# Optimization experiments

Measured on AMD Instinct MI355X. Metric: run time of the kernel, lower is better.

The kernel has to match this reference:

```python
import jax, jax.numpy as jnp
import numpy as np


def setup_inputs() -> dict:
    key = jax.random.key(0)
    k0, k1, k2, k3 = jax.random.split(key, 4)
    B, L, D, H = 8, 4096, 300, 128  # batch, leaves (power of 2), embed dim, hidden
    x = jax.random.normal(k0, (B, L, D), jnp.float32)
    W_leaf = jax.random.normal(k1, (D, 2 * H), jnp.float32) * (1.0 / np.sqrt(D))
    b_leaf = jnp.zeros((2 * H,), jnp.float32)
    W_l = jax.random.normal(k2, (H, 5 * H), jnp.float32) * (1.0 / np.sqrt(H))
    W_r = jax.random.normal(k3, (H, 5 * H), jnp.float32) * (1.0 / np.sqrt(H))
    b = jnp.zeros((5 * H,), jnp.float32)
    return {"x": x, "W_leaf": W_leaf, "b_leaf": b_leaf, "W_l": W_l, "W_r": W_r, "b": b}


def reference(x, W_leaf, b_leaf, W_l, W_r, b):
    """Binary TreeLSTM over a complete tree: leaves -> root.

    x: [B, L, D] leaf embeddings, L a power of 2.
    Leaf transform: linear projection split into (h, c) (SPINN-style).
    REDUCE: 5-gate child-sum-of-two composition.
    Returns root hidden state: [B, H].
    """
    H = W_l.shape[0]
    hc = x @ W_leaf + b_leaf                     # [B, L, 2H]
    h, c = hc[..., :H], hc[..., H:]
    levels = int(np.log2(x.shape[1]))
    for _ in range(levels):                      # level-batched tree reduction
        h_l, h_r = h[:, 0::2], h[:, 1::2]        # [B, n/2, H]
        c_l, c_r = c[:, 0::2], c[:, 1::2]
        gates = h_l @ W_l + h_r @ W_r + b        # [B, n/2, 5H]
        i, fl, fr, o, g = jnp.split(gates, 5, axis=-1)
        c = (jax.nn.sigmoid(fl) * c_l
             + jax.nn.sigmoid(fr) * c_r
             + jax.nn.sigmoid(i) * jnp.tanh(g))
        h = jax.nn.sigmoid(o) * jnp.tanh(c)
    return h[:, 0]                               # root hidden state [B, H]
```

## Files before the change

### kernel.cpp

```cpp
#include <hip/hip_runtime.h>
#include <hip/hip_bf16.h>
#include <math.h>


typedef __attribute__((ext_vector_type(8))) short bfrag8;
typedef __attribute__((ext_vector_type(4))) float f32x4;
typedef __attribute__((ext_vector_type(4))) short s16x4;

__device__ __forceinline__ float sigf(float x) { return 1.0f / (1.0f + __expf(-x)); }
__device__ __forceinline__ short f2bf(float f) {
    __hip_bfloat16 h = __float2bfloat16(f);
    return *reinterpret_cast<short*>(&h);
}
#define GLDS(gp, lp) __builtin_amdgcn_global_load_lds( \
    (const __attribute__((address_space(1))) void*)(gp), \
    (__attribute__((address_space(3))) void*)(lp), 16, 0, 0)

__global__ __launch_bounds__(256) void reorder_kernel(
    const float* __restrict__ W_l, const float* __restrict__ W_r,
    const float* __restrict__ W_leaf,
    short* __restrict__ Wcat_ch, short* __restrict__ Wleaf_ch)
{
    int idx = blockIdx.x * 256 + threadIdx.x;
    if (idx < 163840) {
        int n = idx >> 8, k = idx & 255;
        float v = (k < 128) ? W_l[k * 640 + n] : W_r[(k - 128) * 640 + n];
        Wcat_ch[(((size_t)(k >> 3)) * 640 + n) * 8 + (k & 7)] = f2bf(v);
        return;
    }
    idx -= 163840;
    if (idx < 81920) {
        int n = idx / 320, k = idx - n * 320;
        short v = (k < 300) ? f2bf(W_leaf[k * 256 + n]) : (short)0;
        Wleaf_ch[(((size_t)(k >> 3)) * 256 + n) * 8 + (k & 7)] = v;
    }
}

__global__ __launch_bounds__(256) void convx_kernel(
    const float* __restrict__ x, short* __restrict__ xbf)
{
    __shared__ short Ls[64 * 328];
    const int tid = threadIdx.x;
    const int R0 = blockIdx.x * 64;
    for (int i = tid; i < 64 * 75; i += 256) {
        int r = i / 75, q = i - r * 75;
        f32x4 v = *(const f32x4*)(x + (size_t)(R0 + r) * 300 + q * 4);
        s16x4 o;
        #pragma unroll
        for (int t = 0; t < 4; ++t) o[t] = f2bf(v[t]);
        *(s16x4*)(Ls + r * 328 + q * 4) = o;
    }
    for (int i = tid; i < 64 * 20; i += 256) {
        int r = i / 20, q = i - r * 20;
        Ls[r * 328 + 300 + q] = 0;
    }
    __syncthreads();
    for (int i = tid; i < 40 * 64; i += 256) {
        int c = i >> 6, r = i & 63;
        bfrag8 v = *(const bfrag8*)(Ls + r * 328 + c * 8);
        *(bfrag8*)(xbf + ((size_t)c * 32768 + R0 + r) * 8) = v;
    }
}

__global__ __launch_bounds__(256) void leaf_kernel(
    const short* __restrict__ A, const short* __restrict__ B,
    const float* __restrict__ bleaf,
    short* __restrict__ hD,
    float* __restrict__ cD)
{
    __shared__ short Als[8 * 128 * 8];
    __shared__ short Bls[8 * 128 * 8];
    const int tid  = threadIdx.x;
    const int w    = tid >> 6, lane = tid & 63;
    const int quad = lane >> 4, l16 = lane & 15;
    const int mBlk = blockIdx.x * 128, nBlk = blockIdx.y * 128;
    const int waveM = (w >> 1) * 64, waveN = (w & 1) * 64;

    f32x4 acc[4][4] = {};

    for (int k0 = 0; k0 < 40; k0 += 8) {
        #pragma unroll
        for (int q = 0; q < 4; ++q) {
            int rr = w * 4 + q, cl = rr >> 1, rh = rr & 1;
            GLDS(A + ((size_t)(k0 + cl) * 32768 + mBlk + rh * 64 + lane) * 8,
                 (char*)Als + rr * 1024);
            GLDS(B + ((size_t)(k0 + cl) * 256 + nBlk + rh * 64 + lane) * 8,
                 (char*)Bls + rr * 1024);
        }
        __syncthreads();
        #pragma unroll
        for (int ks = 0; ks < 2; ++ks) {
            int ca = ks * 4 + quad;
            bfrag8 af[4], bf[4];
            #pragma unroll
            for (int i = 0; i < 4; ++i)
                af[i] = *(const bfrag8*)(Als + (ca * 128 + waveM + i * 16 + l16) * 8);
            #pragma unroll
            for (int jn = 0; jn < 4; ++jn)
                bf[jn] = *(const bfrag8*)(Bls + (ca * 128 + waveN + jn * 16 + l16) * 8);
            #pragma unroll
            for (int i = 0; i < 4; ++i)
                #pragma unroll
                for (int jn = 0; jn < 4; ++jn)
                    acc[i][jn] = __builtin_amdgcn_mfma_f32_16x16x32_bf16(
                                     af[i], bf[jn], acc[i][jn], 0, 0, 0);
        }
        __syncthreads();
    }

    #pragma unroll
    for (int i = 0; i < 4; ++i) {
        int row0 = mBlk + waveM + i * 16 + quad * 4;
        #pragma unroll
        for (int jn = 0; jn < 4; ++jn) {
            int col = nBlk + waveN + jn * 16 + l16;
            float bv = bleaf[col];
            #pragma unroll
            for (int rg = 0; rg < 4; ++rg) {
                float v = acc[i][jn][rg] + bv;
                int m = row0 + rg;
                if (nBlk == 0) {
                    int hc = col;
                    hD[(((size_t)((m & 1) * 16 + (hc >> 3))) * 16384 + (m >> 1)) * 8
                       + (hc & 7)] = f2bf(v);
                } else {
                    cD[(size_t)m * 128 + (col - 128)] = v;
                }
            }
        }
    }
}

__global__ __launch_bounds__(256, 2) void level_ws_kernel(
    const short* __restrict__ A,
    const float* __restrict__ cprev,
    const short* __restrict__ Wch,
    const float* __restrict__ bias,
    short* __restrict__ hout, float* __restrict__ cout,
    int M, float* __restrict__ out_final)
{
    __shared__ short Als[32 * 64 * 8];
    const int tid  = threadIdx.x;
    const int w    = tid >> 6, lane = tid & 63;
    const int quad = lane >> 4, l16 = lane & 15;
    const int j  = blockIdx.y;
    const int tb = blockIdx.x * 64;
    const int h  = j * 16 + l16;

    {
        int row = tb + lane; if (row >= M) row = 0;
        #pragma unroll
        for (int s = 0; s < 8; ++s)
            GLDS(A + ((size_t)(s * 4 + w) * M + row) * 8,
                 (char*)Als + (s * 4 + w) * 1024);
    }

    bfrag8 Wfr[5][8];
    #pragma unroll
    for (int g = 0; g < 5; ++g)
        #pragma unroll
        for (int s = 0; s < 8; ++s)
            Wfr[g][s] = *(const bfrag8*)(Wch + ((size_t)(s * 4 + quad) * 640
                                                + g * 128 + h) * 8);
    const float bi  = bias[h],       bfl = bias[128 + h], bfr_ = bias[256 + h];
    const float bo  = bias[384 + h], bg  = bias[512 + h];

    __syncthreads();

    f32x4 acc[5] = {};
    #pragma unroll
    for (int s = 0; s < 8; ++s) {
        bfrag8 af = *(const bfrag8*)(Als + ((s * 4 + quad) * 64 + w * 16 + l16) * 8);
        #pragma unroll
        for (int g = 0; g < 5; ++g)
            acc[g] = __builtin_amdgcn_mfma_f32_16x16x32_bf16(af, Wfr[g][s], acc[g], 0, 0, 0);
    }

    const int Mn = M >> 1;
    #pragma unroll
    for (int rg = 0; rg < 4; ++rg) {
        int m = tb + w * 16 + quad * 4 + rg;
        if (m < M) {
            float gi  = acc[0][rg] + bi;
            float gfl = acc[1][rg] + bfl;
            float gfr = acc[2][rg] + bfr_;
            float go  = acc[3][rg] + bo;
            float gg  = acc[4][rg] + bg;
            float cl  = cprev[(size_t)(2 * m) * 128 + h];
            float cr  = cprev[(size_t)(2 * m + 1) * 128 + h];
            float cn  = sigf(gfl) * cl + sigf(gfr) * cr + sigf(gi) * tanhf(gg);
            float hn  = sigf(go) * tanhf(cn);
            if (out_final) {
                out_final[(size_t)m * 128 + h] = hn;
            } else {
                hout[(((size_t)((m & 1) * 16 + (h >> 3))) * Mn + (m >> 1)) * 8
                     + (h & 7)] = f2bf(hn);
                cout[(size_t)m * 128 + h] = cn;
            }
        }
    }
}

extern "C" void kernel_launch(void* const* d_in, const int* in_sizes, int n_in,
                              void* d_out, int out_size, void* d_ws, size_t ws_size,
                              hipStream_t stream)
{
    const float* x      = (const float*)d_in[0];
    const float* W_leaf = (const float*)d_in[1];
    const float* b_leaf = (const float*)d_in[2];
    const float* W_l    = (const float*)d_in[3];
    const float* W_r    = (const float*)d_in[4];
    const float* b      = (const float*)d_in[5];
    float* out = (float*)d_out;

    char* p = (char*)d_ws;
    short* xbf   = (short*)p; p += (size_t)40 * 32768 * 16;
    short* hA    = (short*)p; p += (size_t)32 * 16384 * 16 + 1024;
    short* hB    = (short*)p; p += (size_t)32 * 8192 * 16 + 1024;
    float* c0    = (float*)p; p += (size_t)32768 * 128 * 4;
    float* c1    = (float*)p; p += (size_t)16384 * 128 * 4;
    short* WcatC = (short*)p; p += (size_t)32 * 640 * 16;
    short* WlfC  = (short*)p; p += (size_t)40 * 256 * 16;

    reorder_kernel<<<960, 256, 0, stream>>>(W_l, W_r, W_leaf, WcatC, WlfC);
    convx_kernel<<<512, 256, 0, stream>>>(x, xbf);
    leaf_kernel<<<dim3(256, 2), 256, 0, stream>>>(xbf, WlfC, b_leaf, hA, c0);

    const short* hin = hA; const float* cin = c0;
    int M = 16384;
    for (int lev = 1; lev <= 12; ++lev) {
        short* ho = (lev & 1) ? hB : hA;
        float* co = (lev & 1) ? c1 : c0;
        float* of = (lev == 12) ? out : nullptr;
        level_ws_kernel<<<dim3((M + 63) / 64, 8), 256, 0, stream>>>(
            hin, cin, WcatC, b, ho, co, M, of);
        hin = ho; cin = co;
        M >>= 1;
    }
}
```

Measured before the change: 207.4 us.

## Fuse tree levels into one persistent cooperative kernel and double-buffer the leaf GEMM

```diff
diff --git a/kernel.cpp b/kernel.cpp
--- a/kernel.cpp
+++ b/kernel.cpp
@@ -1,6 +1,9 @@
 #include <hip/hip_runtime.h>
 #include <hip/hip_bf16.h>
+#include <hip/hip_cooperative_groups.h>
 #include <math.h>
+
+namespace cg = cooperative_groups;
 
 
 typedef __attribute__((ext_vector_type(8))) short bfrag8;
@@ -16,12 +19,38 @@
     (const __attribute__((address_space(1))) void*)(gp), \
     (__attribute__((address_space(3))) void*)(lp), 16, 0, 0)
 
-__global__ __launch_bounds__(256) void reorder_kernel(
+__global__ __launch_bounds__(256) void prep_kernel(
     const float* __restrict__ W_l, const float* __restrict__ W_r,
-    const float* __restrict__ W_leaf,
-    short* __restrict__ Wcat_ch, short* __restrict__ Wleaf_ch)
-{
-    int idx = blockIdx.x * 256 + threadIdx.x;
+    const float* __restrict__ W_leaf, const float* __restrict__ x,
+    short* __restrict__ Wcat_ch, short* __restrict__ Wleaf_ch,
+    short* __restrict__ xbf)
+{
+    __shared__ short Ls[64 * 328];
+    const int tid = threadIdx.x;
+    const int b = blockIdx.x;
+    if (b < 512) {
+        const int R0 = b * 64;
+        for (int i = tid; i < 64 * 75; i += 256) {
+            int r = i / 75, q = i - r * 75;
+            f32x4 v = *(const f32x4*)(x + (size_t)(R0 + r) * 300 + q * 4);
+            s16x4 o;
+            #pragma unroll
+            for (int t = 0; t < 4; ++t) o[t] = f2bf(v[t]);
+            *(s16x4*)(Ls + r * 328 + q * 4) = o;
+        }
+        for (int i = tid; i < 64 * 20; i += 256) {
+            int r = i / 20, q = i - r * 20;
+            Ls[r * 328 + 300 + q] = 0;
+        }
+        __syncthreads();
+        for (int i = tid; i < 40 * 64; i += 256) {
+            int c = i >> 6, r = i & 63;
+            bfrag8 v = *(const bfrag8*)(Ls + r * 328 + c * 8);
+            *(bfrag8*)(xbf + ((size_t)c * 32768 + R0 + r) * 8) = v;
+        }
+        return;
+    }
+    int idx = (b - 512) * 256 + tid;
     if (idx < 163840) {
         int n = idx >> 8, k = idx & 255;
         float v = (k < 128) ? W_l[k * 640 + n] : W_r[(k - 128) * 640 + n];
@@ -36,40 +65,14 @@
     }
 }
 
-__global__ __launch_bounds__(256) void convx_kernel(
-    const float* __restrict__ x, short* __restrict__ xbf)
-{
-    __shared__ short Ls[64 * 328];
-    const int tid = threadIdx.x;
-    const int R0 = blockIdx.x * 64;
-    for (int i = tid; i < 64 * 75; i += 256) {
-        int r = i / 75, q = i - r * 75;
-        f32x4 v = *(const f32x4*)(x + (size_t)(R0 + r) * 300 + q * 4);
-        s16x4 o;
-        #pragma unroll
-        for (int t = 0; t < 4; ++t) o[t] = f2bf(v[t]);
-        *(s16x4*)(Ls + r * 328 + q * 4) = o;
-    }
-    for (int i = tid; i < 64 * 20; i += 256) {
-        int r = i / 20, q = i - r * 20;
-        Ls[r * 328 + 300 + q] = 0;
-    }
-    __syncthreads();
-    for (int i = tid; i < 40 * 64; i += 256) {
-        int c = i >> 6, r = i & 63;
-        bfrag8 v = *(const bfrag8*)(Ls + r * 328 + c * 8);
-        *(bfrag8*)(xbf + ((size_t)c * 32768 + R0 + r) * 8) = v;
-    }
-}
-
-__global__ __launch_bounds__(256) void leaf_kernel(
+__global__ __launch_bounds__(256, 2) void leaf_kernel(
     const short* __restrict__ A, const short* __restrict__ B,
     const float* __restrict__ bleaf,
     short* __restrict__ hD,
     float* __restrict__ cD)
 {
-    __shared__ short Als[8 * 128 * 8];
-    __shared__ short Bls[8 * 128 * 8];
+    __shared__ short Als[2][8 * 128 * 8];
+    __shared__ short Bls[2][8 * 128 * 8];
     const int tid  = threadIdx.x;
     const int w    = tid >> 6, lane = tid & 63;
     const int quad = lane >> 4, l16 = lane & 15;
@@ -78,26 +81,34 @@
 
     f32x4 acc[4][4] = {};
 
-    for (int k0 = 0; k0 < 40; k0 += 8) {
+    auto stage = [&](int k0, int buf) {
         #pragma unroll
         for (int q = 0; q < 4; ++q) {
             int rr = w * 4 + q, cl = rr >> 1, rh = rr & 1;
             GLDS(A + ((size_t)(k0 + cl) * 32768 + mBlk + rh * 64 + lane) * 8,
-                 (char*)Als + rr * 1024);
+                 (char*)Als[buf] + rr * 1024);
             GLDS(B + ((size_t)(k0 + cl) * 256 + nBlk + rh * 64 + lane) * 8,
-                 (char*)Bls + rr * 1024);
-        }
+                 (char*)Bls[buf] + rr * 1024);
+        }
+    };
+
+    stage(0, 0);
+    #pragma unroll
+    for (int s = 0; s < 5; ++s) {
         __syncthreads();
+        if (s < 4) stage((s + 1) * 8, (s + 1) & 1);
+        const short* Ab = Als[s & 1];
+        const short* Bb = Bls[s & 1];
         #pragma unroll
         for (int ks = 0; ks < 2; ++ks) {
             int ca = ks * 4 + quad;
             bfrag8 af[4], bf[4];
             #pragma unroll
             for (int i = 0; i < 4; ++i)
-                af[i] = *(const bfrag8*)(Als + (ca * 128 + waveM + i * 16 + l16) * 8);
+                af[i] = *(const bfrag8*)(Ab + (ca * 128 + waveM + i * 16 + l16) * 8);
             #pragma unroll
             for (int jn = 0; jn < 4; ++jn)
-                bf[jn] = *(const bfrag8*)(Bls + (ca * 128 + waveN + jn * 16 + l16) * 8);
+                bf[jn] = *(const bfrag8*)(Bb + (ca * 128 + waveN + jn * 16 + l16) * 8);
             #pragma unroll
             for (int i = 0; i < 4; ++i)
                 #pragma unroll
@@ -105,7 +116,6 @@
                     acc[i][jn] = __builtin_amdgcn_mfma_f32_16x16x32_bf16(
                                      af[i], bf[jn], acc[i][jn], 0, 0, 0);
         }
-        __syncthreads();
     }
 
     #pragma unroll
@@ -131,73 +141,100 @@
     }
 }
 
-__global__ __launch_bounds__(256, 2) void level_ws_kernel(
-    const short* __restrict__ A,
-    const float* __restrict__ cprev,
+__global__ __launch_bounds__(256, 2) void coop_levels_kernel(
     const short* __restrict__ Wch,
     const float* __restrict__ bias,
-    short* __restrict__ hout, float* __restrict__ cout,
-    int M, float* __restrict__ out_final)
-{
+    short* hA, float* c0, short* hB, float* c1,
+    float* __restrict__ out)
+{
+    cg::grid_group grid = cg::this_grid();
+    __shared__ short Wlds[32 * 80 * 8];
     __shared__ short Als[32 * 64 * 8];
     const int tid  = threadIdx.x;
     const int w    = tid >> 6, lane = tid & 63;
     const int quad = lane >> 4, l16 = lane & 15;
-    const int j  = blockIdx.y;
-    const int tb = blockIdx.x * 64;
+    const int j  = blockIdx.x & 7;
+    const int rs = blockIdx.x >> 3;
     const int h  = j * 16 + l16;
 
-    {
-        int row = tb + lane; if (row >= M) row = 0;
+    #pragma unroll
+    for (int q = 0; q < 10; ++q) {
+        int r = w * 10 + q;
+        int u = r * 64 + lane;
+        int c = u / 80, np = u - c * 80;
+        int g = np >> 4, hh = np & 15;
+        GLDS(Wch + ((size_t)c * 640 + g * 128 + j * 16 + hh) * 8,
+             (char*)Wlds + r * 1024);
+    }
+    __syncthreads();
+    bfrag8 Wfr[5][8];
+    #pragma unroll
+    for (int g = 0; g < 5; ++g)
         #pragma unroll
         for (int s = 0; s < 8; ++s)
-            GLDS(A + ((size_t)(s * 4 + w) * M + row) * 8,
-                 (char*)Als + (s * 4 + w) * 1024);
-    }
-
-    bfrag8 Wfr[5][8];
-    #pragma unroll
-    for (int g = 0; g < 5; ++g)
-        #pragma unroll
-        for (int s = 0; s < 8; ++s)
-            Wfr[g][s] = *(const bfrag8*)(Wch + ((size_t)(s * 4 + quad) * 640
-                                                + g * 128 + h) * 8);
+            Wfr[g][s] = *(const bfrag8*)(Wlds + (((s * 4 + quad) * 80) + g * 16 + l16) * 8);
     const float bi  = bias[h],       bfl = bias[128 + h], bfr_ = bias[256 + h];
     const float bo  = bias[384 + h], bg  = bias[512 + h];
 
-    __syncthreads();
-
-    f32x4 acc[5] = {};
-    #pragma unroll
-    for (int s = 0; s < 8; ++s) {
-        bfrag8 af = *(const bfrag8*)(Als + ((s * 4 + quad) * 64 + w * 16 + l16) * 8);
-        #pragma unroll
-        for (int g = 0; g < 5; ++g)
-            acc[g] = __builtin_amdgcn_mfma_f32_16x16x32_bf16(af, Wfr[g][s], acc[g], 0, 0, 0);
-    }
-
-    const int Mn = M >> 1;
-    #pragma unroll
-    for (int rg = 0; rg < 4; ++rg) {
-        int m = tb + w * 16 + quad * 4 + rg;
-        if (m < M) {
-            float gi  = acc[0][rg] + bi;
-            float gfl = acc[1][rg] + bfl;
-            float gfr = acc[2][rg] + bfr_;
-            float go  = acc[3][rg] + bo;
-            float gg  = acc[4][rg] + bg;
-            float cl  = cprev[(size_t)(2 * m) * 128 + h];
-            float cr  = cprev[(size_t)(2 * m + 1) * 128 + h];
-            float cn  = sigf(gfl) * cl + sigf(gfr) * cr + sigf(gi) * tanhf(gg);
-            float hn  = sigf(go) * tanhf(cn);
-            if (out_final) {
-                out_final[(size_t)m * 128 + h] = hn;
-            } else {
-                hout[(((size_t)((m & 1) * 16 + (h >> 3))) * Mn + (m >> 1)) * 8
-                     + (h & 7)] = f2bf(hn);
-                cout[(size_t)m * 128 + h] = cn;
-            }
-        }
+    const short* hin = hA; const float* cin = c0;
+    short* hout = hB; float* cout = c1;
+    int M = 16384;
+
+    for (int lev = 1; lev <= 12; ++lev) {
+        float* of = (lev == 12) ? out : nullptr;
+        const int Mn = M >> 1;
+        const int T = (M + 63) >> 6;
+        for (int t = rs; t < T; t += 32) {
+            const int tb = t * 64;
+            __syncthreads();
+            {
+                int row = tb + lane; if (row >= M) row = 0;
+                #pragma unroll
+                for (int s = 0; s < 8; ++s)
+                    GLDS(hin + ((size_t)(s * 4 + w) * M + row) * 8,
+                         (char*)Als + (s * 4 + w) * 1024);
+            }
+            __syncthreads();
+
+            f32x4 acc[5] = {};
+            #pragma unroll
+            for (int s = 0; s < 8; ++s) {
+                bfrag8 af = *(const bfrag8*)(Als + ((s * 4 + quad) * 64
+                                                    + w * 16 + l16) * 8);
+                #pragma unroll
+                for (int g = 0; g < 5; ++g)
+                    acc[g] = __builtin_amdgcn_mfma_f32_16x16x32_bf16(
+                                 af, Wfr[g][s], acc[g], 0, 0, 0);
+            }
+
+            #pragma unroll
+            for (int rg = 0; rg < 4; ++rg) {
+                int m = tb + w * 16 + quad * 4 + rg;
+                if (m < M) {
+                    float gi  = acc[0][rg] + bi;
+                    float gfl = acc[1][rg] + bfl;
+                    float gfr = acc[2][rg] + bfr_;
+                    float go  = acc[3][rg] + bo;
+                    float gg  = acc[4][rg] + bg;
+                    float cl  = cin[(size_t)(2 * m) * 128 + h];
+                    float cr  = cin[(size_t)(2 * m + 1) * 128 + h];
+                    float cn  = sigf(gfl) * cl + sigf(gfr) * cr + sigf(gi) * tanhf(gg);
+                    float hn  = sigf(go) * tanhf(cn);
+                    if (of) {
+                        of[(size_t)m * 128 + h] = hn;
+                    } else {
+                        hout[(((size_t)((m & 1) * 16 + (h >> 3))) * Mn + (m >> 1)) * 8
+                             + (h & 7)] = f2bf(hn);
+                        cout[(size_t)m * 128 + h] = cn;
+                    }
+                }
+            }
+        }
+        grid.sync();
+        const short* nh = hin; const float* nc = cin;
+        hin = hout; cin = cout;
+        hout = (short*)nh; cout = (float*)nc;
+        M >>= 1;
     }
 }
 
@@ -222,19 +259,11 @@
     short* WcatC = (short*)p; p += (size_t)32 * 640 * 16;
     short* WlfC  = (short*)p; p += (size_t)40 * 256 * 16;
 
-    reorder_kernel<<<960, 256, 0, stream>>>(W_l, W_r, W_leaf, WcatC, WlfC);
-    convx_kernel<<<512, 256, 0, stream>>>(x, xbf);
+    prep_kernel<<<1472, 256, 0, stream>>>(W_l, W_r, W_leaf, x, WcatC, WlfC, xbf);
     leaf_kernel<<<dim3(256, 2), 256, 0, stream>>>(xbf, WlfC, b_leaf, hA, c0);
 
-    const short* hin = hA; const float* cin = c0;
-    int M = 16384;
-    for (int lev = 1; lev <= 12; ++lev) {
-        short* ho = (lev & 1) ? hB : hA;
-        float* co = (lev & 1) ? c1 : c0;
-        float* of = (lev == 12) ? out : nullptr;
-        level_ws_kernel<<<dim3((M + 63) / 64, 8), 256, 0, stream>>>(
-            hin, cin, WcatC, b, ho, co, M, of);
-        hin = ho; cin = co;
-        M >>= 1;
-    }
-}
+    void* cargs[] = { (void*)&WcatC, (void*)&b, (void*)&hA, (void*)&c0,
+                      (void*)&hB, (void*)&c1, (void*)&out };
+    hipLaunchCooperativeKernel((void*)coop_levels_kernel, dim3(256), dim3(256),
+                               cargs, 0, stream);
+}
```

Result: slower. 540.0 us (+160.4%).
